# Kernel optimization log

Measured on AMD Instinct MI355X. Metric: run time of the kernel, lower is better.

## Reference

```python
import jax, jax.numpy as jnp
import numpy as np

EPS = 1e-7
NUM_NODES = 50000


def setup_inputs() -> dict:
    key = jax.random.key(0)
    k1, k2, k3 = jax.random.split(key, 3)
    n_nodes, n_edges, d = NUM_NODES, 800000, 64
    x = jax.random.normal(k1, (n_nodes, d), dtype=jnp.float32)
    edge_index = jax.random.randint(k2, (2, n_edges), 0, n_nodes, dtype=jnp.int64)
    W = jax.random.normal(k3, (d, d), dtype=jnp.float32) * (1.0 / np.sqrt(d))
    b = jnp.zeros((d,), dtype=jnp.float32)
    beta = jnp.ones((1,), dtype=jnp.float32)
    return {"x": x, "edge_index": edge_index, "W": W, "b": b, "beta": beta}


def _segment_softmax(logits, seg, num_segments):
    # numerically stable softmax over edges grouped by destination node, per channel
    m = jax.ops.segment_max(logits, seg, num_segments=num_segments)  # [N, d]
    m = jnp.where(jnp.isfinite(m), m, 0.0)  # empty segments -> -inf; neutralize
    e = jnp.exp(logits - m[seg])                                      # [E, d]
    denom = jax.ops.segment_sum(e, seg, num_segments=num_segments)    # [N, d]
    return e / (denom[seg] + 1e-16)


def reference(x, edge_index, W, b, beta):
    num_nodes, dim = x.shape
    dst = edge_index[0]
    src = edge_index[1]
    # gather + message encoder (ReLU) + eps
    edge_msg = jax.nn.relu(x[src]) + EPS                               # [E, d]
    # softmax_sg: softmax(beta * msg) per destination segment, beta is a stop-grad scalar
    alpha = _segment_softmax(beta[0] * edge_msg, dst, num_nodes)       # [E, d]
    h = edge_msg * alpha                                               # [E, d]
    # scatter-add aggregation to destination nodes
    agg = jax.ops.segment_sum(h, dst, num_segments=num_nodes)          # [N, d]
    # final dense linear (nn.Linear): agg @ W.T + b
    return agg @ W.T + b
```

## Files before the change

### kernel.cpp

```cpp
#include <hip/hip_runtime.h>
#include <hip/hip_fp16.h>

#define EPS 1e-7f
#define LOG2E 1.4426950408889634f
#define CAPB 1280
#define STG 1792
#define NBMAX 800

typedef _Float16 half8 __attribute__((ext_vector_type(8)));
typedef float f32x4 __attribute__((ext_vector_type(4)));

__global__ __launch_bounds__(512)
void binprep_kernel(const int* __restrict__ dst,
                    const int* __restrict__ src, int E, int NB,
                    const float* __restrict__ x,
                    const float* __restrict__ W,
                    const float* __restrict__ beta, int M,
                    int* __restrict__ ccur,
                    unsigned* __restrict__ packed,
                    unsigned short* __restrict__ tm,
                    unsigned short* __restrict__ Wh,
                    int binBlocks) {
    if ((int)blockIdx.x < binBlocks) {
        __shared__ int lc[NBMAX];
        __shared__ int lbase[NBMAX];
        int tid = threadIdx.x;
        for (int i = tid; i < NB; i += 512) lc[i] = 0;
        __syncthreads();
        int e0 = blockIdx.x * 4096;
        int bb[8], rr[8];
        unsigned pk[8];
        #pragma unroll
        for (int i = 0; i < 8; ++i) {
            int e = e0 + i * 512 + tid;
            bb[i] = 0; rr[i] = 0; pk[i] = 0;
            if (e < E) {
                int d = dst[e];
                bb[i] = d >> 6;
                pk[i] = ((unsigned)(d & 63) << 16) | (unsigned)src[e];
                rr[i] = atomicAdd(&lc[bb[i]], 1);
            }
        }
        __syncthreads();
        for (int i = tid; i < NB; i += 512) {
            int c = lc[i];
            if (c) lbase[i] = i * CAPB + atomicAdd(&ccur[i], c);
        }
        __syncthreads();
        #pragma unroll
        for (int i = 0; i < 8; ++i) {
            int e = e0 + i * 512 + tid;
            if (e < E) {
                int pos = lbase[bb[i]] + rr[i];
                if (pos < (bb[i] + 1) * CAPB)
                    packed[pos] = pk[i];
            }
        }
    } else {
        int blk = blockIdx.x - binBlocks;
        int tid = threadIdx.x;
        if (blk == 0) {
            #pragma unroll
            for (int j = 0; j < 8; ++j) {
                int i = tid * 8 + j;
                Wh[i] = __half_as_ushort(__float2half_rn(W[i]));
            }
        }
        const float btl = beta[0] * LOG2E;
        const unsigned short sent = __half_as_ushort(__float2half_rn(-1000.f));
        #pragma unroll
        for (int p = 0; p < 4; ++p) {
            int i = blk * 8192 + p * 2048 + tid * 4;
            if (i < M) {
                float4 v = *(const float4*)&x[i];
                ushort4 o;
                o.x = __half_as_ushort(__float2half_rn((fmaxf(v.x, 0.f) + EPS) * btl));
                o.y = __half_as_ushort(__float2half_rn((fmaxf(v.y, 0.f) + EPS) * btl));
                o.z = __half_as_ushort(__float2half_rn((fmaxf(v.z, 0.f) + EPS) * btl));
                o.w = __half_as_ushort(__float2half_rn((fmaxf(v.w, 0.f) + EPS) * btl));
                *(ushort4*)&tm[i] = o;
            } else if (i < M + 64) {
                ushort4 o; o.x = o.y = o.z = o.w = sent;
                *(ushort4*)&tm[i] = o;
            }
        }
    }
}

__global__ __launch_bounds__(512)
void gatherlin_kernel(const unsigned* __restrict__ packed,
                      const int* __restrict__ ccur,
                      const unsigned short* __restrict__ tm,
                      const unsigned short* __restrict__ Wh,
                      const float* __restrict__ bias,
                      const float* __restrict__ beta,
                      float* __restrict__ out, int N) {
    __shared__ unsigned stage_pk[CAPB];
    __shared__ unsigned short stage16[STG];
    __shared__ short aggS[64 * 72];
    __shared__ int lc[64], nstart[64], lcur[64];

    const int tid = threadIdx.x;
    const int b = blockIdx.x;
    const unsigned short sentid = (unsigned short)N;

    int len = ccur[b];
    if (len > CAPB) len = CAPB;
    const int rs = b * CAPB;

    if (tid < 64) lc[tid] = 0;
    __syncthreads();

    for (int i = tid; i < len; i += 512) {
        unsigned u = packed[rs + i];
        stage_pk[i] = u;
        atomicAdd(&lc[u >> 16], 1);
    }
    __syncthreads();

    if (tid < 64) {
        int c8 = (lc[tid] + 7) & ~7;
        int incl = c8;
        #pragma unroll
        for (int d = 1; d < 64; d <<= 1) {
            int t = __shfl_up(incl, d, 64);
            if (tid >= d) incl += t;
        }
        nstart[tid] = incl - c8;
        lcur[tid] = incl - c8;
    }
    __syncthreads();

    for (int i = tid; i < len; i += 512) {
        unsigned u = stage_pk[i];
        int pos = atomicAdd(&lcur[u >> 16], 1);
        stage16[pos] = (unsigned short)(u & 0xffffu);
    }
    if (tid < 64) {
        int c = lc[tid];
        int c8 = (c + 7) & ~7;
        int s = nstart[tid];
        for (int j = c; j < c8; ++j) stage16[s + j] = sentid;
    }
    __syncthreads();

    const int g   = tid >> 4;
    const int l16 = tid & 15;
    const int chb = l16 << 3;
    const unsigned char* tb = (const unsigned char*)tm;
    const float scale = 0.6931471805599453f / beta[0];

    #pragma unroll 1
    for (int sub = 0; sub < 2; ++sub) {
        const int nl = (g << 1) | sub;
        const int start = nstart[nl];
        const int cnt = lc[nl];

        float s1x = 0.f, s1y = 0.f, s1z = 0.f, s1w = 0.f;
        float s2x = 0.f, s2y = 0.f, s2z = 0.f, s2w = 0.f;

        #pragma unroll 1
        for (int k = 0; k < cnt; k += 8) {
            uint4 e8 = *(const uint4*)&stage16[start + k];
            int r0 = (int)(e8.x & 0xffffu) << 7;
            int r1 = (int)(e8.x >> 16) << 7;
            int r2 = (int)(e8.y & 0xffffu) << 7;
            int r3 = (int)(e8.y >> 16) << 7;
            int r4 = (int)(e8.z & 0xffffu) << 7;
            int r5 = (int)(e8.z >> 16) << 7;
            int r6 = (int)(e8.w & 0xffffu) << 7;
            int r7 = (int)(e8.w >> 16) << 7;
            uint2 u0 = *(const uint2*)(tb + (r0 + chb));
            uint2 u1 = *(const uint2*)(tb + (r1 + chb));
            uint2 u2 = *(const uint2*)(tb + (r2 + chb));
            uint2 u3 = *(const uint2*)(tb + (r3 + chb));
            uint2 u4 = *(const uint2*)(tb + (r4 + chb));
            uint2 u5 = *(const uint2*)(tb + (r5 + chb));
            uint2 u6 = *(const uint2*)(tb + (r6 + chb));
            uint2 u7 = *(const uint2*)(tb + (r7 + chb));
            #define ACC(u) { \
                float m0 = __half2float(__ushort_as_half((unsigned short)(u.x & 0xffffu))); \
                float m1 = __half2float(__ushort_as_half((unsigned short)(u.x >> 16))); \
                float m2 = __half2float(__ushort_as_half((unsigned short)(u.y & 0xffffu))); \
                float m3 = __half2float(__ushort_as_half((unsigned short)(u.y >> 16))); \
                float e0 = exp2f(m0), e1 = exp2f(m1); \
                float e2 = exp2f(m2), e3 = exp2f(m3); \
                s1x += e0; s2x = fmaf(m0, e0, s2x); \
                s1y += e1; s2y = fmaf(m1, e1, s2y); \
                s1z += e2; s2z = fmaf(m2, e2, s2z); \
                s1w += e3; s2w = fmaf(m3, e3, s2w); }
            ACC(u0); ACC(u1); ACC(u2); ACC(u3);
            ACC(u4); ACC(u5); ACC(u6); ACC(u7);
            #undef ACC
        }

        float gx = __fdividef(s2x, s1x + 1e-16f) * scale;
        float gy = __fdividef(s2y, s1y + 1e-16f) * scale;
        float gz = __fdividef(s2z, s1z + 1e-16f) * scale;
        float gw = __fdividef(s2w, s1w + 1e-16f) * scale;
        uint2 o;
        o.x = (unsigned)__half_as_ushort(__float2half_rn(gx)) |
              ((unsigned)__half_as_ushort(__float2half_rn(gy)) << 16);
        o.y = (unsigned)__half_as_ushort(__float2half_rn(gz)) |
              ((unsigned)__half_as_ushort(__float2half_rn(gw)) << 16);
        *(uint2*)((unsigned char*)aggS + nl * 144 + chb) = o;
    }
    __syncthreads();

    const int wave = tid >> 6;
    const int lane = tid & 63;
    const int quarter = lane >> 4;
    const int wl16 = lane & 15;
    const int oc0 = (wave & 3) << 4;
    const unsigned char* ab = (const unsigned char*)aggS;
    const unsigned char* wr =
        (const unsigned char*)Wh + (((size_t)(oc0 + wl16)) << 7) + quarter * 16;
    half8 b0 = *(const half8*)(wr);
    half8 b1 = *(const half8*)(wr + 64);
    const float bv = bias[oc0 + wl16];
    #pragma unroll
    for (int s = 0; s < 2; ++s) {
        const int tt = ((wave >> 2) << 1) + s;
        half8 a0 = *(const half8*)(ab + (tt * 16 + wl16) * 144 + quarter * 16);
        half8 a1 = *(const half8*)(ab + (tt * 16 + wl16) * 144 + 64 + quarter * 16);
        f32x4 acc = (f32x4){0.f, 0.f, 0.f, 0.f};
        acc = __builtin_amdgcn_mfma_f32_16x16x32_f16(a0, b0, acc, 0, 0, 0);
        acc = __builtin_amdgcn_mfma_f32_16x16x32_f16(a1, b1, acc, 0, 0, 0);
        #pragma unroll
        for (int r = 0; r < 4; ++r) {
            int nd = b * 64 + tt * 16 + quarter * 4 + r;
            if (nd < N)
                out[((size_t)nd << 6) + oc0 + wl16] = acc[r] + bv;
        }
    }
}

extern "C" void kernel_launch(void* const* d_in, const int* in_sizes, int n_in,
                              void* d_out, int out_size, void* d_ws, size_t ws_size,
                              hipStream_t stream) {
    const float* x    = (const float*)d_in[0];
    const int*   ei   = (const int*)d_in[1];
    const float* W    = (const float*)d_in[2];
    const float* b    = (const float*)d_in[3];
    const float* beta = (const float*)d_in[4];
    float* out = (float*)d_out;

    const int N = in_sizes[0] / 64;
    const int E = in_sizes[1] / 2;
    const int* dst = ei;
    const int* src = ei + E;
    const int NB = (N + 63) >> 6;
    const int M = N * 64;

    auto align = [](size_t v) { return (v + 255) & ~(size_t)255; };
    size_t off = 0;
    char* ws = (char*)d_ws;
    int* ccur = (int*)(ws + off);         off += align((size_t)NB * 4);
    unsigned* packed = (unsigned*)(ws + off);
    off += align((size_t)NB * CAPB * 4);
    unsigned short* tm = (unsigned short*)(ws + off);
    off += align(((size_t)N + 1) * 64 * 2);
    unsigned short* Wh = (unsigned short*)(ws + off);
    off += align(64 * 64 * 2);

    const int binBlocks  = (E + 4095) / 4096;
    const int prepBlocks = (M + 64 + 8191) / 8192;
    hipMemsetAsync(ccur, 0, (size_t)NB * 4, stream);
    binprep_kernel<<<binBlocks + prepBlocks, 512, 0, stream>>>(
        dst, src, E, NB, x, W, beta, M, ccur, packed, tm, Wh, binBlocks);
    gatherlin_kernel<<<NB, 512, 0, stream>>>(packed, ccur, tm, Wh, b, beta,
                                             out, N);
}
```

Before: 115.5 us.

## Fuse binning, prep and gather-linear into one persistent kernel with grid barrier

Merges the two kernels into a single persistent kernel launched with a bounded grid. A software grid-wide barrier (an atomic counter in the workspace, zeroed by the existing memset) separates the binning/prep phase from the gather/softmax/linear phase. Each block loops over edge chunks and node bins in grid-stride fashion. This removes one kernel launch and the gap between launches, but adds barrier spin cost, and correctness relies on all G blocks being co-resident.

```diff
diff --git a/kernel.cpp b/kernel.cpp
--- a/kernel.cpp
+++ b/kernel.cpp
@@ -10,228 +10,236 @@
 typedef _Float16 half8 __attribute__((ext_vector_type(8)));
 typedef float f32x4 __attribute__((ext_vector_type(4)));
 
-__global__ __launch_bounds__(512)
-void binprep_kernel(const int* __restrict__ dst,
-                    const int* __restrict__ src, int E, int NB,
-                    const float* __restrict__ x,
-                    const float* __restrict__ W,
-                    const float* __restrict__ beta, int M,
-                    int* __restrict__ ccur,
-                    unsigned* __restrict__ packed,
-                    unsigned short* __restrict__ tm,
-                    unsigned short* __restrict__ Wh,
-                    int binBlocks) {
-    if ((int)blockIdx.x < binBlocks) {
-        __shared__ int lc[NBMAX];
-        __shared__ int lbase[NBMAX];
-        int tid = threadIdx.x;
-        for (int i = tid; i < NB; i += 512) lc[i] = 0;
-        __syncthreads();
-        int e0 = blockIdx.x * 4096;
-        int bb[8], rr[8];
-        unsigned pk[8];
-        #pragma unroll
-        for (int i = 0; i < 8; ++i) {
+__global__ __launch_bounds__(512, 4)
+void genconv_fused(const int* __restrict__ dst,
+                   const int* __restrict__ src, int E, int NB,
+                   const float* __restrict__ x,
+                   const float* __restrict__ W,
+                   const float* __restrict__ beta, int M,
+                   unsigned* __restrict__ bar,
+                   int* __restrict__ ccur,
+                   unsigned* __restrict__ packed,
+                   unsigned short* __restrict__ tm,
+                   unsigned short* __restrict__ Wh,
+                   const float* __restrict__ bias,
+                   float* __restrict__ out, int N, int G) {
+    __shared__ int lcA[NBMAX];
+    __shared__ int lbaseA[NBMAX];
+    __shared__ unsigned stage_pk[CAPB];
+    __shared__ unsigned short stage16[STG];
+    __shared__ short aggS[64 * 72];
+    __shared__ int lc[64], nstart[64], lcur[64];
+
+    const int tid = threadIdx.x;
+    const int b = blockIdx.x;
+
+    for (int e0 = b * 2048; e0 < E; e0 += G * 2048) {
+        for (int i = tid; i < NB; i += 512) lcA[i] = 0;
+        __syncthreads();
+        int bb[4], rr[4];
+        unsigned pk[4];
+        #pragma unroll
+        for (int i = 0; i < 4; ++i) {
             int e = e0 + i * 512 + tid;
             bb[i] = 0; rr[i] = 0; pk[i] = 0;
             if (e < E) {
                 int d = dst[e];
                 bb[i] = d >> 6;
                 pk[i] = ((unsigned)(d & 63) << 16) | (unsigned)src[e];
-                rr[i] = atomicAdd(&lc[bb[i]], 1);
+                rr[i] = atomicAdd(&lcA[bb[i]], 1);
             }
         }
         __syncthreads();
         for (int i = tid; i < NB; i += 512) {
-            int c = lc[i];
-            if (c) lbase[i] = i * CAPB + atomicAdd(&ccur[i], c);
-        }
-        __syncthreads();
-        #pragma unroll
-        for (int i = 0; i < 8; ++i) {
+            int c = lcA[i];
+            if (c) lbaseA[i] = i * CAPB + atomicAdd(&ccur[i], c);
+        }
+        __syncthreads();
+        #pragma unroll
+        for (int i = 0; i < 4; ++i) {
             int e = e0 + i * 512 + tid;
             if (e < E) {
-                int pos = lbase[bb[i]] + rr[i];
+                int pos = lbaseA[bb[i]] + rr[i];
                 if (pos < (bb[i] + 1) * CAPB)
                     packed[pos] = pk[i];
             }
         }
-    } else {
-        int blk = blockIdx.x - binBlocks;
-        int tid = threadIdx.x;
-        if (blk == 0) {
-            #pragma unroll
-            for (int j = 0; j < 8; ++j) {
-                int i = tid * 8 + j;
-                Wh[i] = __half_as_ushort(__float2half_rn(W[i]));
-            }
-        }
+        __syncthreads();
+    }
+
+    if (b == 0) {
+        #pragma unroll
+        for (int j = 0; j < 8; ++j) {
+            int i = tid * 8 + j;
+            Wh[i] = __half_as_ushort(__float2half_rn(W[i]));
+        }
+    }
+    {
         const float btl = beta[0] * LOG2E;
         const unsigned short sent = __half_as_ushort(__float2half_rn(-1000.f));
-        #pragma unroll
-        for (int p = 0; p < 4; ++p) {
-            int i = blk * 8192 + p * 2048 + tid * 4;
-            if (i < M) {
-                float4 v = *(const float4*)&x[i];
-                ushort4 o;
-                o.x = __half_as_ushort(__float2half_rn((fmaxf(v.x, 0.f) + EPS) * btl));
-                o.y = __half_as_ushort(__float2half_rn((fmaxf(v.y, 0.f) + EPS) * btl));
-                o.z = __half_as_ushort(__float2half_rn((fmaxf(v.z, 0.f) + EPS) * btl));
-                o.w = __half_as_ushort(__float2half_rn((fmaxf(v.w, 0.f) + EPS) * btl));
-                *(ushort4*)&tm[i] = o;
-            } else if (i < M + 64) {
-                ushort4 o; o.x = o.y = o.z = o.w = sent;
-                *(ushort4*)&tm[i] = o;
-            }
-        }
-    }
-}
-
-__global__ __launch_bounds__(512)
-void gatherlin_kernel(const unsigned* __restrict__ packed,
-                      const int* __restrict__ ccur,
-                      const unsigned short* __restrict__ tm,
-                      const unsigned short* __restrict__ Wh,
-                      const float* __restrict__ bias,
-                      const float* __restrict__ beta,
-                      float* __restrict__ out, int N) {
-    __shared__ unsigned stage_pk[CAPB];
-    __shared__ unsigned short stage16[STG];
-    __shared__ short aggS[64 * 72];
-    __shared__ int lc[64], nstart[64], lcur[64];
-
-    const int tid = threadIdx.x;
-    const int b = blockIdx.x;
+        for (int i0 = b * 8192; i0 < M + 64; i0 += G * 8192) {
+            #pragma unroll
+            for (int p = 0; p < 4; ++p) {
+                int i = i0 + p * 2048 + tid * 4;
+                if (i < M) {
+                    float4 v = *(const float4*)&x[i];
+                    ushort4 o;
+                    o.x = __half_as_ushort(__float2half_rn((fmaxf(v.x, 0.f) + EPS) * btl));
+                    o.y = __half_as_ushort(__float2half_rn((fmaxf(v.y, 0.f) + EPS) * btl));
+                    o.z = __half_as_ushort(__float2half_rn((fmaxf(v.z, 0.f) + EPS) * btl));
+                    o.w = __half_as_ushort(__float2half_rn((fmaxf(v.w, 0.f) + EPS) * btl));
+                    *(ushort4*)&tm[i] = o;
+                } else if (i < M + 64) {
+                    ushort4 o; o.x = o.y = o.z = o.w = sent;
+                    *(ushort4*)&tm[i] = o;
+                }
+            }
+        }
+    }
+
+    __threadfence();
+    __syncthreads();
+    if (tid == 0) {
+        __hip_atomic_fetch_add(bar, 1u, __ATOMIC_ACQ_REL,
+                               __HIP_MEMORY_SCOPE_AGENT);
+        while (__hip_atomic_load(bar, __ATOMIC_ACQUIRE,
+                                 __HIP_MEMORY_SCOPE_AGENT) < (unsigned)G)
+            __builtin_amdgcn_s_sleep(2);
+    }
+    __syncthreads();
+
     const unsigned short sentid = (unsigned short)N;
-
-    int len = ccur[b];
-    if (len > CAPB) len = CAPB;
-    const int rs = b * CAPB;
-
-    if (tid < 64) lc[tid] = 0;
-    __syncthreads();
-
-    for (int i = tid; i < len; i += 512) {
-        unsigned u = packed[rs + i];
-        stage_pk[i] = u;
-        atomicAdd(&lc[u >> 16], 1);
-    }
-    __syncthreads();
-
-    if (tid < 64) {
-        int c8 = (lc[tid] + 7) & ~7;
-        int incl = c8;
-        #pragma unroll
-        for (int d = 1; d < 64; d <<= 1) {
-            int t = __shfl_up(incl, d, 64);
-            if (tid >= d) incl += t;
-        }
-        nstart[tid] = incl - c8;
-        lcur[tid] = incl - c8;
-    }
-    __syncthreads();
-
-    for (int i = tid; i < len; i += 512) {
-        unsigned u = stage_pk[i];
-        int pos = atomicAdd(&lcur[u >> 16], 1);
-        stage16[pos] = (unsigned short)(u & 0xffffu);
-    }
-    if (tid < 64) {
-        int c = lc[tid];
-        int c8 = (c + 7) & ~7;
-        int s = nstart[tid];
-        for (int j = c; j < c8; ++j) stage16[s + j] = sentid;
-    }
-    __syncthreads();
-
-    const int g   = tid >> 4;
-    const int l16 = tid & 15;
-    const int chb = l16 << 3;
-    const unsigned char* tb = (const unsigned char*)tm;
-    const float scale = 0.6931471805599453f / beta[0];
-
-    #pragma unroll 1
-    for (int sub = 0; sub < 2; ++sub) {
-        const int nl = (g << 1) | sub;
-        const int start = nstart[nl];
-        const int cnt = lc[nl];
-
-        float s1x = 0.f, s1y = 0.f, s1z = 0.f, s1w = 0.f;
-        float s2x = 0.f, s2y = 0.f, s2z = 0.f, s2w = 0.f;
+    for (int bk = b; bk < NB; bk += G) {
+        if (tid < 64) lc[tid] = 0;
+        __syncthreads();
+
+        int len = ccur[bk];
+        if (len > CAPB) len = CAPB;
+        const int rs = bk * CAPB;
+
+        for (int i = tid; i < len; i += 512) {
+            unsigned u = packed[rs + i];
+            stage_pk[i] = u;
+            atomicAdd(&lc[u >> 16], 1);
+        }
+        __syncthreads();
+
+        if (tid < 64) {
+            int c8 = (lc[tid] + 7) & ~7;
+            int incl = c8;
+            #pragma unroll
+            for (int d = 1; d < 64; d <<= 1) {
+                int t = __shfl_up(incl, d, 64);
+                if (tid >= d) incl += t;
+            }
+            nstart[tid] = incl - c8;
+            lcur[tid] = incl - c8;
+        }
+        __syncthreads();
+
+        for (int i = tid; i < len; i += 512) {
+            unsigned u = stage_pk[i];
+            int pos = atomicAdd(&lcur[u >> 16], 1);
+            stage16[pos] = (unsigned short)(u & 0xffffu);
+        }
+        if (tid < 64) {
+            int c = lc[tid];
+            int c8 = (c + 7) & ~7;
+            int s = nstart[tid];
+            for (int j = c; j < c8; ++j) stage16[s + j] = sentid;
+        }
+        __syncthreads();
+
+        const int g   = tid >> 4;
+        const int l16 = tid & 15;
+        const int chb = l16 << 3;
+        const unsigned char* tb = (const unsigned char*)tm;
+        const float scale = 0.6931471805599453f / beta[0];
 
         #pragma unroll 1
-        for (int k = 0; k < cnt; k += 8) {
-            uint4 e8 = *(const uint4*)&stage16[start + k];
-            int r0 = (int)(e8.x & 0xffffu) << 7;
-            int r1 = (int)(e8.x >> 16) << 7;
-            int r2 = (int)(e8.y & 0xffffu) << 7;
-            int r3 = (int)(e8.y >> 16) << 7;
-            int r4 = (int)(e8.z & 0xffffu) << 7;
-            int r5 = (int)(e8.z >> 16) << 7;
-            int r6 = (int)(e8.w & 0xffffu) << 7;
-            int r7 = (int)(e8.w >> 16) << 7;
-            uint2 u0 = *(const uint2*)(tb + (r0 + chb));
-            uint2 u1 = *(const uint2*)(tb + (r1 + chb));
-            uint2 u2 = *(const uint2*)(tb + (r2 + chb));
-            uint2 u3 = *(const uint2*)(tb + (r3 + chb));
-            uint2 u4 = *(const uint2*)(tb + (r4 + chb));
-            uint2 u5 = *(const uint2*)(tb + (r5 + chb));
-            uint2 u6 = *(const uint2*)(tb + (r6 + chb));
-            uint2 u7 = *(const uint2*)(tb + (r7 + chb));
-            #define ACC(u) { \
-                float m0 = __half2float(__ushort_as_half((unsigned short)(u.x & 0xffffu))); \
-                float m1 = __half2float(__ushort_as_half((unsigned short)(u.x >> 16))); \
-                float m2 = __half2float(__ushort_as_half((unsigned short)(u.y & 0xffffu))); \
-                float m3 = __half2float(__ushort_as_half((unsigned short)(u.y >> 16))); \
-                float e0 = exp2f(m0), e1 = exp2f(m1); \
-                float e2 = exp2f(m2), e3 = exp2f(m3); \
-                s1x += e0; s2x = fmaf(m0, e0, s2x); \
-                s1y += e1; s2y = fmaf(m1, e1, s2y); \
-                s1z += e2; s2z = fmaf(m2, e2, s2z); \
-                s1w += e3; s2w = fmaf(m3, e3, s2w); }
-            ACC(u0); ACC(u1); ACC(u2); ACC(u3);
-            ACC(u4); ACC(u5); ACC(u6); ACC(u7);
-            #undef ACC
-        }
-
-        float gx = __fdividef(s2x, s1x + 1e-16f) * scale;
-        float gy = __fdividef(s2y, s1y + 1e-16f) * scale;
-        float gz = __fdividef(s2z, s1z + 1e-16f) * scale;
-        float gw = __fdividef(s2w, s1w + 1e-16f) * scale;
-        uint2 o;
-        o.x = (unsigned)__half_as_ushort(__float2half_rn(gx)) |
-              ((unsigned)__half_as_ushort(__float2half_rn(gy)) << 16);
-        o.y = (unsigned)__half_as_ushort(__float2half_rn(gz)) |
-              ((unsigned)__half_as_ushort(__float2half_rn(gw)) << 16);
-        *(uint2*)((unsigned char*)aggS + nl * 144 + chb) = o;
-    }
-    __syncthreads();
-
-    const int wave = tid >> 6;
-    const int lane = tid & 63;
-    const int quarter = lane >> 4;
-    const int wl16 = lane & 15;
-    const int oc0 = (wave & 3) << 4;
-    const unsigned char* ab = (const unsigned char*)aggS;
-    const unsigned char* wr =
-        (const unsigned char*)Wh + (((size_t)(oc0 + wl16)) << 7) + quarter * 16;
-    half8 b0 = *(const half8*)(wr);
-    half8 b1 = *(const half8*)(wr + 64);
-    const float bv = bias[oc0 + wl16];
-    #pragma unroll
-    for (int s = 0; s < 2; ++s) {
-        const int tt = ((wave >> 2) << 1) + s;
-        half8 a0 = *(const half8*)(ab + (tt * 16 + wl16) * 144 + quarter * 16);
-        half8 a1 = *(const half8*)(ab + (tt * 16 + wl16) * 144 + 64 + quarter * 16);
-        f32x4 acc = (f32x4){0.f, 0.f, 0.f, 0.f};
-        acc = __builtin_amdgcn_mfma_f32_16x16x32_f16(a0, b0, acc, 0, 0, 0);
-        acc = __builtin_amdgcn_mfma_f32_16x16x32_f16(a1, b1, acc, 0, 0, 0);
-        #pragma unroll
-        for (int r = 0; r < 4; ++r) {
-            int nd = b * 64 + tt * 16 + quarter * 4 + r;
-            if (nd < N)
-                out[((size_t)nd << 6) + oc0 + wl16] = acc[r] + bv;
-        }
+        for (int sub = 0; sub < 2; ++sub) {
+            const int nl = (g << 1) | sub;
+            const int start = nstart[nl];
+            const int cnt = lc[nl];
+
+            float s1x = 0.f, s1y = 0.f, s1z = 0.f, s1w = 0.f;
+            float s2x = 0.f, s2y = 0.f, s2z = 0.f, s2w = 0.f;
+
+            #pragma unroll 1
+            for (int k = 0; k < cnt; k += 8) {
+                uint4 e8 = *(const uint4*)&stage16[start + k];
+                int r0 = (int)(e8.x & 0xffffu) << 7;
+                int r1 = (int)(e8.x >> 16) << 7;
+                int r2 = (int)(e8.y & 0xffffu) << 7;
+                int r3 = (int)(e8.y >> 16) << 7;
+                int r4 = (int)(e8.z & 0xffffu) << 7;
+                int r5 = (int)(e8.z >> 16) << 7;
+                int r6 = (int)(e8.w & 0xffffu) << 7;
+                int r7 = (int)(e8.w >> 16) << 7;
+                uint2 u0 = *(const uint2*)(tb + (r0 + chb));
+                uint2 u1 = *(const uint2*)(tb + (r1 + chb));
+                uint2 u2 = *(const uint2*)(tb + (r2 + chb));
+                uint2 u3 = *(const uint2*)(tb + (r3 + chb));
+                uint2 u4 = *(const uint2*)(tb + (r4 + chb));
+                uint2 u5 = *(const uint2*)(tb + (r5 + chb));
+                uint2 u6 = *(const uint2*)(tb + (r6 + chb));
+                uint2 u7 = *(const uint2*)(tb + (r7 + chb));
+                #define ACC(u) { \
+                    float m0 = __half2float(__ushort_as_half((unsigned short)(u.x & 0xffffu))); \
+                    float m1 = __half2float(__ushort_as_half((unsigned short)(u.x >> 16))); \
+                    float m2 = __half2float(__ushort_as_half((unsigned short)(u.y & 0xffffu))); \
+                    float m3 = __half2float(__ushort_as_half((unsigned short)(u.y >> 16))); \
+                    float e0 = exp2f(m0), e1 = exp2f(m1); \
+                    float e2 = exp2f(m2), e3 = exp2f(m3); \
+                    s1x += e0; s2x = fmaf(m0, e0, s2x); \
+                    s1y += e1; s2y = fmaf(m1, e1, s2y); \
+                    s1z += e2; s2z = fmaf(m2, e2, s2z); \
+                    s1w += e3; s2w = fmaf(m3, e3, s2w); }
+                ACC(u0); ACC(u1); ACC(u2); ACC(u3);
+                ACC(u4); ACC(u5); ACC(u6); ACC(u7);
+                #undef ACC
+            }
+
+            float gx = __fdividef(s2x, s1x + 1e-16f) * scale;
+            float gy = __fdividef(s2y, s1y + 1e-16f) * scale;
+            float gz = __fdividef(s2z, s1z + 1e-16f) * scale;
+            float gw = __fdividef(s2w, s1w + 1e-16f) * scale;
+            uint2 o;
+            o.x = (unsigned)__half_as_ushort(__float2half_rn(gx)) |
+                  ((unsigned)__half_as_ushort(__float2half_rn(gy)) << 16);
+            o.y = (unsigned)__half_as_ushort(__float2half_rn(gz)) |
+                  ((unsigned)__half_as_ushort(__float2half_rn(gw)) << 16);
+            *(uint2*)((unsigned char*)aggS + nl * 144 + chb) = o;
+        }
+        __syncthreads();
+
+        const int wave = tid >> 6;
+        const int lane = tid & 63;
+        const int quarter = lane >> 4;
+        const int wl16 = lane & 15;
+        const int oc0 = (wave & 3) << 4;
+        const unsigned char* ab = (const unsigned char*)aggS;
+        const unsigned char* wr =
+            (const unsigned char*)Wh + (((size_t)(oc0 + wl16)) << 7) + quarter * 16;
+        half8 b0 = *(const half8*)(wr);
+        half8 b1 = *(const half8*)(wr + 64);
+        const float bv = bias[oc0 + wl16];
+        #pragma unroll
+        for (int s = 0; s < 2; ++s) {
+            const int tt = ((wave >> 2) << 1) + s;
+            half8 a0 = *(const half8*)(ab + (tt * 16 + wl16) * 144 + quarter * 16);
+            half8 a1 = *(const half8*)(ab + (tt * 16 + wl16) * 144 + 64 + quarter * 16);
+            f32x4 acc = (f32x4){0.f, 0.f, 0.f, 0.f};
+            acc = __builtin_amdgcn_mfma_f32_16x16x32_f16(a0, b0, acc, 0, 0, 0);
+            acc = __builtin_amdgcn_mfma_f32_16x16x32_f16(a1, b1, acc, 0, 0, 0);
+            #pragma unroll
+            for (int r = 0; r < 4; ++r) {
+                int nd = bk * 64 + tt * 16 + quarter * 4 + r;
+                if (nd < N)
+                    out[((size_t)nd << 6) + oc0 + wl16] = acc[r] + bv;
+            }
+        }
+        __syncthreads();
     }
 }
 
@@ -255,7 +263,8 @@
     auto align = [](size_t v) { return (v + 255) & ~(size_t)255; };
     size_t off = 0;
     char* ws = (char*)d_ws;
-    int* ccur = (int*)(ws + off);         off += align((size_t)NB * 4);
+    unsigned* bar = (unsigned*)(ws + off);      off += align(256);
+    int* ccur = (int*)(ws + off);               off += align((size_t)NB * 4);
     unsigned* packed = (unsigned*)(ws + off);
     off += align((size_t)NB * CAPB * 4);
     unsigned short* tm = (unsigned short*)(ws + off);
@@ -263,11 +272,13 @@
     unsigned short* Wh = (unsigned short*)(ws + off);
     off += align(64 * 64 * 2);
 
-    const int binBlocks  = (E + 4095) / 4096;
-    const int prepBlocks = (M + 64 + 8191) / 8192;
-    hipMemsetAsync(ccur, 0, (size_t)NB * 4, stream);
-    binprep_kernel<<<binBlocks + prepBlocks, 512, 0, stream>>>(
-        dst, src, E, NB, x, W, beta, M, ccur, packed, tm, Wh, binBlocks);
-    gatherlin_kernel<<<NB, 512, 0, stream>>>(packed, ccur, tm, Wh, b, beta,
-                                             out, N);
+    int G = (E + 2047) / 2048;
+    int Gt = (M + 64 + 8191) / 8192;
+    if (Gt > G) G = Gt;
+    if (G > 512) G = 512;
+
+    hipMemsetAsync(ws, 0, align(256) + align((size_t)NB * 4), stream);
+    genconv_fused<<<G, 512, 0, stream>>>(dst, src, E, NB, x, W, beta, M,
+                                         bar, ccur, packed, tm, Wh, b,
+                                         out, N, G);
 }
```

Result: slower. 279.6 us (+142.1%).
